# Kernel optimization log

Measured on AMD Instinct MI355X. Metric: run time of the kernel, lower is better.

The kernel has to match this reference:

```python
import jax, jax.numpy as jnp
import numpy as np

N_NODES = 100000
N_EDGES = 1250000
N_PAIRS = 200000
IN_DIM = 128
HID = 64
N_LAYERS = 3


def setup_inputs() -> dict:
    key = jax.random.key(0)
    ks = jax.random.split(key, 16)
    x = jax.random.normal(ks[0], (N_NODES, IN_DIM), dtype=jnp.float32)
    edge_index = jax.random.randint(ks[1], (2, N_EDGES), 0, N_NODES, dtype=jnp.int64)
    pair_index = jax.random.randint(ks[2], (N_PAIRS, 2), 0, N_NODES, dtype=jnp.int64)
    s_in = 1.0 / np.sqrt(IN_DIM)
    s_h = 1.0 / np.sqrt(HID)
    s_2h = 1.0 / np.sqrt(2 * HID)
    enc_W = jax.random.uniform(ks[3], (IN_DIM, HID), jnp.float32, -s_in, s_in)
    enc_b = jax.random.uniform(ks[4], (HID,), jnp.float32, -s_in, s_in)
    # SAGEConv params per layer: lin_l (neighbors, with bias), lin_r (root, no bias)
    Wl = jax.random.uniform(ks[5], (N_LAYERS, HID, HID), jnp.float32, -s_h, s_h)
    bl = jax.random.uniform(ks[6], (N_LAYERS, HID), jnp.float32, -s_h, s_h)
    Wr = jax.random.uniform(ks[7], (N_LAYERS, HID, HID), jnp.float32, -s_h, s_h)
    # predictor MLP: Linear(2h -> h), ReLU, Linear(h -> 1)
    W1 = jax.random.uniform(ks[8], (2 * HID, HID), jnp.float32, -s_2h, s_2h)
    b1 = jax.random.uniform(ks[9], (HID,), jnp.float32, -s_2h, s_2h)
    W2 = jax.random.uniform(ks[10], (HID, 1), jnp.float32, -s_h, s_h)
    b2 = jax.random.uniform(ks[11], (1,), jnp.float32, -s_h, s_h)
    return {"x": x, "edge_index": edge_index, "pair_index": pair_index,
            "enc_W": enc_W, "enc_b": enc_b, "Wl": Wl, "bl": bl, "Wr": Wr,
            "W1": W1, "b1": b1, "W2": W2, "b2": b2}


def reference(x, edge_index, pair_index, enc_W, enc_b, Wl, bl, Wr, W1, b1, W2, b2):
    src, dst = edge_index[0], edge_index[1]
    n = x.shape[0]
    # neighbor counts for mean aggregation (empty neighborhoods -> 0, matching PyG)
    deg = jax.ops.segment_sum(jnp.ones((src.shape[0],), x.dtype), dst, num_segments=n)
    inv_deg = jnp.where(deg > 0, 1.0 / jnp.maximum(deg, 1.0), 0.0)[:, None]  # [N,1]
    # node encoder: Linear + ReLU
    h = jax.nn.relu(x @ enc_W + enc_b)  # [N, HID]
    for i in range(Wl.shape[0]):
        # scatter-mean of source features onto destinations
        agg = jax.ops.segment_sum(h[src], dst, num_segments=n) * inv_deg  # [N, HID]
        h = jax.nn.relu(agg @ Wl[i] + bl[i] + h @ Wr[i])
        # dropout is identity in eval mode
    z = jnp.concatenate([h[pair_index[:, 0]], h[pair_index[:, 1]]], axis=1)  # [P, 2*HID]
    out = (jax.nn.relu(z @ W1 + b1) @ W2 + b2)[:, 0]  # [P]
    return out
```

## Files before the change

kernel.cpp:

```cpp
#include <hip/hip_runtime.h>
#include <hip/hip_fp16.h>
#include <cstdint>
#include <cstddef>

#define N_NODES_C 100000
#define N_EDGES_C 1250000
#define N_PAIRS_C 200000
#define IN_DIM_C 128
#define HID_C 64

#define NB_S 256
#define BSH 9
#define NPB 512
#define NBKT 196
#define SEG_CAP 8192

typedef _Float16 f16x8 __attribute__((ext_vector_type(8)));
typedef float f32x4 __attribute__((ext_vector_type(4)));


#define SCAN_TPB 256
#define SCAN_IPT 4
#define SCAN_ELEMS 1024

__global__ void k_scan_partial(const int* __restrict__ in, int* __restrict__ outp,
                               int* __restrict__ blocksums, int n) {
    __shared__ int sd[SCAN_TPB];
    int tid = threadIdx.x;
    int base = blockIdx.x * SCAN_ELEMS + tid * SCAN_IPT;
    int v[SCAN_IPT]; int s = 0;
    for (int k = 0; k < SCAN_IPT; k++) { int idx = base + k; v[k] = (idx < n) ? in[idx] : 0; s += v[k]; }
    sd[tid] = s;
    __syncthreads();
    for (int off = 1; off < SCAN_TPB; off <<= 1) {
        int t = (tid >= off) ? sd[tid - off] : 0;
        __syncthreads();
        sd[tid] += t;
        __syncthreads();
    }
    int excl = sd[tid] - s;
    for (int k = 0; k < SCAN_IPT; k++) { int idx = base + k; if (idx < n) outp[idx] = excl; excl += v[k]; }
    if (tid == SCAN_TPB - 1) blocksums[blockIdx.x] = sd[tid];
}

__global__ void k_scan_blocks(int* __restrict__ bs, int nb) {
    __shared__ int sd[128];
    int t = threadIdx.x;
    int v = (t < nb) ? bs[t] : 0;
    sd[t] = v;
    __syncthreads();
    for (int off = 1; off < 128; off <<= 1) {
        int u = (t >= off) ? sd[t - off] : 0;
        __syncthreads();
        sd[t] += u;
        __syncthreads();
    }
    if (t < nb) bs[t] = sd[t] - v;
}

__global__ void k_scan_addg(int* __restrict__ arr, const int* __restrict__ bs, int n) {
    int i = blockIdx.x * blockDim.x + threadIdx.x;
    if (i < n) arr[i] += bs[i >> 10];
}


__global__ __launch_bounds__(256) void k_hist(const int* __restrict__ dst,
                                              int* __restrict__ histT, int e) {
    __shared__ int lh[NBKT];
    int tid = threadIdx.x, k = blockIdx.x;
    if (tid < NBKT) lh[tid] = 0;
    __syncthreads();
    int chunk = (e + NB_S - 1) / NB_S;
    int i0 = k * chunk, i1 = min(i0 + chunk, e);
    for (int i = i0 + tid; i < i1; i += 256) atomicAdd(&lh[dst[i] >> BSH], 1);
    __syncthreads();
    if (tid < NBKT) histT[tid * NB_S + k] = lh[tid];
}

__global__ __launch_bounds__(256) void k_scatter(const int* __restrict__ edges,
                                                 const int* __restrict__ offs,
                                                 int2* __restrict__ staging, int e) {
    __shared__ int cur[NBKT];
    int tid = threadIdx.x, k = blockIdx.x;
    if (tid < NBKT) cur[tid] = offs[tid * NB_S + k];
    __syncthreads();
    int chunk = (e + NB_S - 1) / NB_S;
    int i0 = k * chunk, i1 = min(i0 + chunk, e);
    for (int i = i0 + tid; i < i1; i += 256) {
        int s = edges[i];
        int d = edges[e + i];
        int p = atomicAdd(&cur[d >> BSH], 1);
        staging[p] = make_int2(s, d);
    }
}

__global__ __launch_bounds__(256) void k_bucket_fill(const int2* __restrict__ staging,
        const int* __restrict__ offs, int* __restrict__ rowptr,
        float* __restrict__ invd, int* __restrict__ adj, int n, int e) {
    __shared__ int ldeg[NPB];
    __shared__ int lrow[NPB];
    __shared__ int ps[256];
    __shared__ int lseg[SEG_CAP];
    int tid = threadIdx.x, b = blockIdx.x;
    int n0 = b << BSH;
    int nn = min(NPB, n - n0);
    int segBeg = offs[b * NB_S];
    int segEnd = (b == NBKT - 1) ? e : offs[(b + 1) * NB_S];

    ldeg[tid] = 0; ldeg[tid + 256] = 0;
    __syncthreads();
    for (int i = segBeg + tid; i < segEnd; i += 256)
        atomicAdd(&ldeg[staging[i].y - n0], 1);
    __syncthreads();

    int a0 = ldeg[2 * tid], a1 = ldeg[2 * tid + 1];
    int s = a0 + a1;
    ps[tid] = s;
    __syncthreads();
    for (int off = 1; off < 256; off <<= 1) {
        int t = (tid >= off) ? ps[tid - off] : 0;
        __syncthreads();
        ps[tid] += t;
        __syncthreads();
    }
    int excl = ps[tid] - s;
    lrow[2 * tid] = excl;
    lrow[2 * tid + 1] = excl + a0;
    __syncthreads();

    for (int j = tid; j < nn; j += 256) {
        rowptr[n0 + j] = segBeg + lrow[j];
        int d = ldeg[j];
        invd[n0 + j] = (d > 0) ? (1.0f / (float)d) : 0.0f;
    }
    if (b == NBKT - 1 && tid == 0) rowptr[n] = e;
    __syncthreads();

    for (int i = segBeg + tid; i < segEnd; i += 256) {
        int2 ed = staging[i];
        int p = atomicAdd(&lrow[ed.y - n0], 1);
        if (p < SEG_CAP) lseg[p] = ed.x;
        else adj[segBeg + p] = ed.x;
    }
    __syncthreads();

    int m = segEnd - segBeg; if (m > SEG_CAP) m = SEG_CAP;
    for (int p = tid; p < m; p += 256) adj[segBeg + p] = lseg[p];
}


__global__ __launch_bounds__(256) void k_aggregate(const int* __restrict__ rowptr,
        const int* __restrict__ adj, const float* __restrict__ invd,
        const __half* __restrict__ hin16, __half* __restrict__ agg16, int n) {
    int wid = threadIdx.x >> 6, lane = threadIdx.x & 63;
    int node0 = (blockIdx.x * 4 + wid) * 8;
    if (node0 >= n) return;
    const int q = lane >> 3;
    const int c8 = (lane & 7) * 8;
    int node = node0 + q;
    bool valid = node < n;
    int nodec = valid ? node : n - 1;
    int beg = rowptr[nodec], end = rowptr[nodec + 1];
    float a0 = 0.f, a1 = 0.f, a2 = 0.f, a3 = 0.f;
    float a4 = 0.f, a5 = 0.f, a6 = 0.f, a7 = 0.f;
    for (int e = beg; e < end; e += 8) {
        int idx[8];
        #pragma unroll
        for (int j = 0; j < 8; ++j) {
            int ee = e + j;
            idx[j] = adj[ee < end ? ee : end - 1];
        }
        float4 raw[8];
        #pragma unroll
        for (int j = 0; j < 8; ++j)
            raw[j] = *(const float4*)&hin16[(size_t)idx[j] * HID_C + c8];
        #pragma unroll
        for (int j = 0; j < 8; ++j) {
            union { float4 f; __half2 h[4]; } u;
            u.f = raw[j];
            float2 f0 = __half22float2(u.h[0]);
            float2 f1 = __half22float2(u.h[1]);
            float2 f2 = __half22float2(u.h[2]);
            float2 f3 = __half22float2(u.h[3]);
            bool in = (e + j < end);
            a0 += in ? f0.x : 0.f;  a1 += in ? f0.y : 0.f;
            a2 += in ? f1.x : 0.f;  a3 += in ? f1.y : 0.f;
            a4 += in ? f2.x : 0.f;  a5 += in ? f2.y : 0.f;
            a6 += in ? f3.x : 0.f;  a7 += in ? f3.y : 0.f;
        }
    }
    if (valid) {
        float s = invd[node];
        union { float4 f; __half2 h[4]; } o;
        o.h[0] = __floats2half2_rn(a0 * s, a1 * s);
        o.h[1] = __floats2half2_rn(a2 * s, a3 * s);
        o.h[2] = __floats2half2_rn(a4 * s, a5 * s);
        o.h[3] = __floats2half2_rn(a6 * s, a7 * s);
        *(float4*)&agg16[(size_t)node * HID_C + c8] = o.f;
    }
}


__device__ __forceinline__ float4 ld4(const float* p) { return *(const float4*)p; }


template<int SRC>
__global__ __launch_bounds__(256, 2) void k_mm(
    const float* __restrict__ A1f,
    const __half* __restrict__ A1h, const __half* __restrict__ A2h,
    const float* __restrict__ Ws1, const float* __restrict__ Ws2,
    const float* __restrict__ bias,
    __half* __restrict__ out16, int nrows)
{
    __shared__ __half Ah[128 * 128];
    __shared__ __half Bt[64 * 128];
    const int t = threadIdx.x;
    const int g0 = blockIdx.x * 128;

    #pragma unroll
    for (int p = 0; p < 8; ++p) {
        int li = p * 256 + t;
        int r = li >> 4;
        int o = li & 15;
        int g = g0 + r; if (g > nrows - 1) g = nrows - 1;
        f16x8 v;
        if (SRC == 0) {
            const float* src = A1f + (size_t)g * 128 + o * 8;
            float4 f0 = ld4(src), f1 = ld4(src + 4);
            v[0] = (_Float16)f0.x; v[1] = (_Float16)f0.y;
            v[2] = (_Float16)f0.z; v[3] = (_Float16)f0.w;
            v[4] = (_Float16)f1.x; v[5] = (_Float16)f1.y;
            v[6] = (_Float16)f1.z; v[7] = (_Float16)f1.w;
        } else {
            const __half* src = (o < 8) ? (A1h + (size_t)g * 64 + o * 8)
                                        : (A2h + (size_t)g * 64 + (o - 8) * 8);
            v = *(const f16x8*)src;
        }
        *(f16x8*)&Ah[r * 128 + (o ^ (r & 15)) * 8] = v;
    }
    #pragma unroll
    for (int p = 0; p < 32; ++p) {
        int li = p * 256 + t;
        int c = li & 63;
        int k = li >> 6;
        float wv;
        if (SRC == 0) wv = Ws1[k * 64 + c];
        else          wv = (k < 64) ? Ws1[k * 64 + c] : Ws2[(k - 64) * 64 + c];
        Bt[c * 128 + (((k >> 3) ^ (c & 15)) * 8) + (k & 7)] = __float2half(wv);
    }
    __syncthreads();

    const int lane = t & 63;
    const int wid = t >> 6;
    const int R = wid * 32;
    const int lr = lane & 15;
    const int lk = lane >> 4;

    f32x4 acc[2][4];
    #pragma unroll
    for (int fr = 0; fr < 2; ++fr)
        #pragma unroll
        for (int fc = 0; fc < 4; ++fc)
            acc[fr][fc] = (f32x4){0.f, 0.f, 0.f, 0.f};

    #pragma unroll
    for (int ks = 0; ks < 4; ++ks) {
        int o = ks * 4 + lk;
        f16x8 af0, af1;
        {
            int r0 = R + lr;
            int r1 = R + 16 + lr;
            af0 = *(const f16x8*)&Ah[r0 * 128 + (o ^ (r0 & 15)) * 8];
            af1 = *(const f16x8*)&Ah[r1 * 128 + (o ^ (r1 & 15)) * 8];
        }
        #pragma unroll
        for (int fc = 0; fc < 4; ++fc) {
            int c = fc * 16 + lr;
            f16x8 bf = *(const f16x8*)&Bt[c * 128 + (o ^ (c & 15)) * 8];
            acc[0][fc] = __builtin_amdgcn_mfma_f32_16x16x32_f16(af0, bf, acc[0][fc], 0, 0, 0);
            acc[1][fc] = __builtin_amdgcn_mfma_f32_16x16x32_f16(af1, bf, acc[1][fc], 0, 0, 0);
        }
    }

    float bv[4];
    #pragma unroll
    for (int fc = 0; fc < 4; ++fc) bv[fc] = bias[fc * 16 + lr];
    #pragma unroll
    for (int fr = 0; fr < 2; ++fr) {
        #pragma unroll
        for (int j = 0; j < 4; ++j) {
            int gr = g0 + R + fr * 16 + lk * 4 + j;
            if (gr < nrows) {
                #pragma unroll
                for (int fc = 0; fc < 4; ++fc) {
                    int col = fc * 16 + lr;
                    float v = fmaxf(acc[fr][fc][j] + bv[fc], 0.f);
                    out16[(size_t)gr * 64 + col] = __float2half(v);
                }
            }
        }
    }
}


__global__ __launch_bounds__(256, 2) void k_uvm(
    const __half* __restrict__ H16, const float* __restrict__ W1,
    __half* __restrict__ U16, __half* __restrict__ V16, int nrows)
{
    __shared__ __half Ah[128 * 64];
    __shared__ __half Bt[128 * 64];
    const int t = threadIdx.x;
    const int g0 = blockIdx.x * 128;

    #pragma unroll
    for (int p = 0; p < 4; ++p) {
        int li = p * 256 + t;
        int r = li >> 3;
        int o = li & 7;
        int g = g0 + r; if (g > nrows - 1) g = nrows - 1;
        f16x8 v = *(const f16x8*)&H16[(size_t)g * 64 + o * 8];
        *(f16x8*)&Ah[r * 64 + (o ^ (r & 7)) * 8] = v;
    }
    #pragma unroll
    for (int p = 0; p < 32; ++p) {
        int li = p * 256 + t;
        int c = li & 127;
        int k = li >> 7;
        float wv = (c < 64) ? W1[k * 64 + c] : W1[(64 + k) * 64 + (c - 64)];
        Bt[c * 64 + (((k >> 3) ^ (c & 7)) * 8) + (k & 7)] = __float2half(wv);
    }
    __syncthreads();

    const int lane = t & 63;
    const int wid = t >> 6;
    const int R = wid * 32;
    const int lr = lane & 15;
    const int lk = lane >> 4;

    f32x4 acc[2][8];
    #pragma unroll
    for (int fr = 0; fr < 2; ++fr)
        #pragma unroll
        for (int fc = 0; fc < 8; ++fc)
            acc[fr][fc] = (f32x4){0.f, 0.f, 0.f, 0.f};

    #pragma unroll
    for (int ks = 0; ks < 2; ++ks) {
        int o = ks * 4 + lk;
        int r0 = R + lr, r1 = R + 16 + lr;
        f16x8 af0 = *(const f16x8*)&Ah[r0 * 64 + (o ^ (r0 & 7)) * 8];
        f16x8 af1 = *(const f16x8*)&Ah[r1 * 64 + (o ^ (r1 & 7)) * 8];
        #pragma unroll
        for (int fc = 0; fc < 8; ++fc) {
            int c = fc * 16 + lr;
            f16x8 bf = *(const f16x8*)&Bt[c * 64 + (o ^ (c & 7)) * 8];
            acc[0][fc] = __builtin_amdgcn_mfma_f32_16x16x32_f16(af0, bf, acc[0][fc], 0, 0, 0);
            acc[1][fc] = __builtin_amdgcn_mfma_f32_16x16x32_f16(af1, bf, acc[1][fc], 0, 0, 0);
        }
    }

    #pragma unroll
    for (int fr = 0; fr < 2; ++fr) {
        #pragma unroll
        for (int j = 0; j < 4; ++j) {
            int gr = g0 + R + fr * 16 + lk * 4 + j;
            if (gr < nrows) {
                #pragma unroll
                for (int fc = 0; fc < 8; ++fc) {
                    int col = fc * 16 + lr;
                    __half v = __float2half(acc[fr][fc][j]);
                    if (col < 64) U16[(size_t)gr * 64 + col] = v;
                    else          V16[(size_t)gr * 64 + (col - 64)] = v;
                }
            }
        }
    }
}

__global__ __launch_bounds__(256) void k_pred(
    const __half* __restrict__ U16, const __half* __restrict__ V16,
    const int* __restrict__ pidx, const float* __restrict__ b1,
    const float* __restrict__ W2, const float* __restrict__ b2,
    float* __restrict__ outp, int np)
{
    const int t = threadIdx.x;
    const int lg = t & 15;
    const int p = blockIdx.x * 16 + (t >> 4);
    float4 bv = ld4(b1 + lg * 4);
    float4 wv = ld4(W2 + lg * 4);
    if (p >= np) return;
    int2 ab = ((const int2*)pidx)[p];
    float2 ur = *(const float2*)&U16[(size_t)ab.x * 64 + lg * 4];
    float2 vr = *(const float2*)&V16[(size_t)ab.y * 64 + lg * 4];
    union { float f; __half2 h; } u0, u1, v0, v1;
    u0.f = ur.x; u1.f = ur.y; v0.f = vr.x; v1.f = vr.y;
    float2 ua = __half22float2(u0.h), ub = __half22float2(u1.h);
    float2 va = __half22float2(v0.h), vb = __half22float2(v1.h);
    float zx = fmaxf(ua.x + va.x + bv.x, 0.f);
    float zy = fmaxf(ua.y + va.y + bv.y, 0.f);
    float zz = fmaxf(ub.x + vb.x + bv.z, 0.f);
    float zw = fmaxf(ub.y + vb.y + bv.w, 0.f);
    float s = zx * wv.x + zy * wv.y + zz * wv.z + zw * wv.w;
    s += __shfl_down(s, 8, 16);
    s += __shfl_down(s, 4, 16);
    s += __shfl_down(s, 2, 16);
    s += __shfl_down(s, 1, 16);
    if (lg == 0) outp[p] = s + b2[0];
}


extern "C" void kernel_launch(void* const* d_in, const int* in_sizes, int n_in,
                              void* d_out, int out_size, void* d_ws, size_t ws_size,
                              hipStream_t stream) {
    const float* x    = (const float*)d_in[0];
    const int*   edges= (const int*)d_in[1];
    const int*   pair = (const int*)d_in[2];
    const float* encW = (const float*)d_in[3];
    const float* encb = (const float*)d_in[4];
    const float* Wl   = (const float*)d_in[5];
    const float* bl   = (const float*)d_in[6];
    const float* Wr   = (const float*)d_in[7];
    const float* W1   = (const float*)d_in[8];
    const float* b1   = (const float*)d_in[9];
    const float* W2   = (const float*)d_in[10];
    const float* b2   = (const float*)d_in[11];
    float* out = (float*)d_out;

    const int N = N_NODES_C, E = N_EDGES_C, P = N_PAIRS_C;
    const int* dst = edges + E;
    const int M = NBKT * NB_S;

    char* w = (char*)d_ws;
    auto alloc = [&](size_t bytes) { char* p = w; w += (bytes + 255) & ~(size_t)255; return p; };
    int*   rowptr = (int*)alloc((size_t)(N + 1) * 4);
    int*   histT  = (int*)alloc((size_t)M * 4);
    int*   offs   = (int*)alloc((size_t)M * 4);
    int*   bsums  = (int*)alloc(128 * 4);
    float* invd   = (float*)alloc((size_t)N * 4);
    int*   adj    = (int*)alloc((size_t)E * 4);
    int2*  staging= (int2*)alloc((size_t)E * 8);
    __half* h16a  = (__half*)alloc((size_t)N * HID_C * 2);
    __half* h16b  = (__half*)alloc((size_t)N * HID_C * 2);
    __half* agg16 = (__half*)alloc((size_t)N * HID_C * 2);
    __half* U16   = (__half*)alloc((size_t)N * HID_C * 2);
    __half* V16   = (__half*)alloc((size_t)N * HID_C * 2);

    int nscan = (M + SCAN_ELEMS - 1) / SCAN_ELEMS;

    hipLaunchKernelGGL(k_hist, dim3(NB_S), dim3(256), 0, stream, dst, histT, E);
    hipLaunchKernelGGL(k_scan_partial, dim3(nscan), dim3(SCAN_TPB), 0, stream, histT, offs, bsums, M);
    hipLaunchKernelGGL(k_scan_blocks, dim3(1), dim3(128), 0, stream, bsums, nscan);
    hipLaunchKernelGGL(k_scan_addg, dim3((M + 255) / 256), dim3(256), 0, stream, offs, bsums, M);
    hipLaunchKernelGGL(k_scatter, dim3(NB_S), dim3(256), 0, stream, edges, offs, staging, E);
    hipLaunchKernelGGL(k_bucket_fill, dim3(NBKT), dim3(256), 0, stream, staging, offs, rowptr, invd, adj, N, E);

    const int NB128 = (N + 127) / 128;

    k_mm<0><<<dim3(NB128), dim3(256), 0, stream>>>(
        x, nullptr, nullptr, encW, nullptr, encb, h16a, N);

    __half* h16c = h16a; __half* h16n = h16b;
    for (int l = 0; l < 3; l++) {
        hipLaunchKernelGGL(k_aggregate, dim3((N + 31) / 32), dim3(256), 0, stream,
                           rowptr, adj, invd, h16c, agg16, N);
        k_mm<1><<<dim3(NB128), dim3(256), 0, stream>>>(
            nullptr, agg16, h16c, Wl + (size_t)l * 64 * 64, Wr + (size_t)l * 64 * 64,
            bl + (size_t)l * 64, h16n, N);
        __half* t16 = h16c; h16c = h16n; h16n = t16;
    }

    const int NB_UV = (N + 127) / 128;
    hipLaunchKernelGGL(k_uvm, dim3(NB_UV), dim3(256), 0, stream, h16c, W1, U16, V16, N);
    hipLaunchKernelGGL(k_pred, dim3((P + 15) / 16), dim3(256), 0, stream,
                       U16, V16, pair, b1, W2, b2, out, P);
}
```

Baseline: 303.0 us.

## Fuse last SAGE layer with predictor U/V projection and single-block scan

Replaces the three-kernel prefix scan with a single 1024-thread block scan, removing two launches. Fuses the final SAGE layer's matmul (agg·Wl + h·Wr + bias, ReLU) with the W1 split projection into one kernel. The intermediate h stays in shared memory instead of being written to and reread from global. The single-block scan serialises roughly 50K elements on one CU, which may cost more than the launches it removes.

```diff
diff --git a/kernel.cpp b/kernel.cpp
--- a/kernel.cpp
+++ b/kernel.cpp
@@ -19,48 +19,27 @@
 typedef float f32x4 __attribute__((ext_vector_type(4)));
 
 
-#define SCAN_TPB 256
-#define SCAN_IPT 4
-#define SCAN_ELEMS 1024
-
-__global__ void k_scan_partial(const int* __restrict__ in, int* __restrict__ outp,
-                               int* __restrict__ blocksums, int n) {
-    __shared__ int sd[SCAN_TPB];
+__global__ __launch_bounds__(1024) void k_scan_full(const int* __restrict__ in,
+                                                    int* __restrict__ outp, int n) {
+    __shared__ int sd[1024];
     int tid = threadIdx.x;
-    int base = blockIdx.x * SCAN_ELEMS + tid * SCAN_IPT;
-    int v[SCAN_IPT]; int s = 0;
-    for (int k = 0; k < SCAN_IPT; k++) { int idx = base + k; v[k] = (idx < n) ? in[idx] : 0; s += v[k]; }
+    int ipt = (n + 1023) >> 10;
+    int base = tid * ipt;
+    int s = 0;
+    for (int k = 0; k < ipt; ++k) { int idx = base + k; if (idx < n) s += in[idx]; }
     sd[tid] = s;
     __syncthreads();
-    for (int off = 1; off < SCAN_TPB; off <<= 1) {
-        int t = (tid >= off) ? sd[tid - off] : 0;
+    for (int off = 1; off < 1024; off <<= 1) {
+        int tv = (tid >= off) ? sd[tid - off] : 0;
         __syncthreads();
-        sd[tid] += t;
+        sd[tid] += tv;
         __syncthreads();
     }
     int excl = sd[tid] - s;
-    for (int k = 0; k < SCAN_IPT; k++) { int idx = base + k; if (idx < n) outp[idx] = excl; excl += v[k]; }
-    if (tid == SCAN_TPB - 1) blocksums[blockIdx.x] = sd[tid];
-}
-
-__global__ void k_scan_blocks(int* __restrict__ bs, int nb) {
-    __shared__ int sd[128];
-    int t = threadIdx.x;
-    int v = (t < nb) ? bs[t] : 0;
-    sd[t] = v;
-    __syncthreads();
-    for (int off = 1; off < 128; off <<= 1) {
-        int u = (t >= off) ? sd[t - off] : 0;
-        __syncthreads();
-        sd[t] += u;
-        __syncthreads();
-    }
-    if (t < nb) bs[t] = sd[t] - v;
-}
-
-__global__ void k_scan_addg(int* __restrict__ arr, const int* __restrict__ bs, int n) {
-    int i = blockIdx.x * blockDim.x + threadIdx.x;
-    if (i < n) arr[i] += bs[i >> 10];
+    for (int k = 0; k < ipt; ++k) {
+        int idx = base + k;
+        if (idx < n) { int v = in[idx]; outp[idx] = excl; excl += v; }
+    }
 }
 
 
@@ -303,31 +282,35 @@
 }
 
 
-__global__ __launch_bounds__(256, 2) void k_uvm(
-    const __half* __restrict__ H16, const float* __restrict__ W1,
+__global__ __launch_bounds__(256, 2) void k_mm_uv(
+    const __half* __restrict__ A1h, const __half* __restrict__ A2h,
+    const float* __restrict__ Ws1, const float* __restrict__ Ws2,
+    const float* __restrict__ bias, const float* __restrict__ W1p,
     __half* __restrict__ U16, __half* __restrict__ V16, int nrows)
 {
-    __shared__ __half Ah[128 * 64];
-    __shared__ __half Bt[128 * 64];
+    __shared__ __half Ah[128 * 128];
+    __shared__ __half Bt[64 * 128];
     const int t = threadIdx.x;
     const int g0 = blockIdx.x * 128;
 
     #pragma unroll
-    for (int p = 0; p < 4; ++p) {
+    for (int p = 0; p < 8; ++p) {
         int li = p * 256 + t;
-        int r = li >> 3;
-        int o = li & 7;
+        int r = li >> 4;
+        int o = li & 15;
         int g = g0 + r; if (g > nrows - 1) g = nrows - 1;
-        f16x8 v = *(const f16x8*)&H16[(size_t)g * 64 + o * 8];
-        *(f16x8*)&Ah[r * 64 + (o ^ (r & 7)) * 8] = v;
+        const __half* src = (o < 8) ? (A1h + (size_t)g * 64 + o * 8)
+                                    : (A2h + (size_t)g * 64 + (o - 8) * 8);
+        f16x8 v = *(const f16x8*)src;
+        *(f16x8*)&Ah[r * 128 + (o ^ (r & 15)) * 8] = v;
     }
     #pragma unroll
     for (int p = 0; p < 32; ++p) {
         int li = p * 256 + t;
-        int c = li & 127;
-        int k = li >> 7;
-        float wv = (c < 64) ? W1[k * 64 + c] : W1[(64 + k) * 64 + (c - 64)];
-        Bt[c * 64 + (((k >> 3) ^ (c & 7)) * 8) + (k & 7)] = __float2half(wv);
+        int c = li & 63;
+        int k = li >> 6;
+        float wv = (k < 64) ? Ws1[k * 64 + c] : Ws2[(k - 64) * 64 + c];
+        Bt[c * 128 + (((k >> 3) ^ (c & 15)) * 8) + (k & 7)] = __float2half(wv);
     }
     __syncthreads();
 
@@ -337,12 +320,64 @@
     const int lr = lane & 15;
     const int lk = lane >> 4;
 
-    f32x4 acc[2][8];
+    f32x4 acc[2][4];
     #pragma unroll
     for (int fr = 0; fr < 2; ++fr)
         #pragma unroll
+        for (int fc = 0; fc < 4; ++fc)
+            acc[fr][fc] = (f32x4){0.f, 0.f, 0.f, 0.f};
+
+    #pragma unroll
+    for (int ks = 0; ks < 4; ++ks) {
+        int o = ks * 4 + lk;
+        int r0 = R + lr, r1 = R + 16 + lr;
+        f16x8 af0 = *(const f16x8*)&Ah[r0 * 128 + (o ^ (r0 & 15)) * 8];
+        f16x8 af1 = *(const f16x8*)&Ah[r1 * 128 + (o ^ (r1 & 15)) * 8];
+        #pragma unroll
+        for (int fc = 0; fc < 4; ++fc) {
+            int c = fc * 16 + lr;
+            f16x8 bf = *(const f16x8*)&Bt[c * 128 + (o ^ (c & 15)) * 8];
+            acc[0][fc] = __builtin_amdgcn_mfma_f32_16x16x32_f16(af0, bf, acc[0][fc], 0, 0, 0);
+            acc[1][fc] = __builtin_amdgcn_mfma_f32_16x16x32_f16(af1, bf, acc[1][fc], 0, 0, 0);
+        }
+    }
+
+    float bv[4];
+    #pragma unroll
+    for (int fc = 0; fc < 4; ++fc) bv[fc] = bias[fc * 16 + lr];
+
+    __syncthreads();
+
+    #pragma unroll
+    for (int fr = 0; fr < 2; ++fr) {
+        #pragma unroll
+        for (int j = 0; j < 4; ++j) {
+            int lrow = R + fr * 16 + lk * 4 + j;
+            #pragma unroll
+            for (int fc = 0; fc < 4; ++fc) {
+                int col = fc * 16 + lr;
+                float v = fmaxf(acc[fr][fc][j] + bv[fc], 0.f);
+                int o = col >> 3;
+                Ah[lrow * 64 + ((o ^ (lrow & 7)) * 8) + (col & 7)] = __float2half(v);
+            }
+        }
+    }
+    #pragma unroll
+    for (int p = 0; p < 32; ++p) {
+        int li = p * 256 + t;
+        int c = li & 127;
+        int k = li >> 7;
+        float wv = (c < 64) ? W1p[k * 64 + c] : W1p[(64 + k) * 64 + (c - 64)];
+        Bt[c * 64 + (((k >> 3) ^ (c & 7)) * 8) + (k & 7)] = __float2half(wv);
+    }
+    __syncthreads();
+
+    f32x4 acc2[2][8];
+    #pragma unroll
+    for (int fr = 0; fr < 2; ++fr)
+        #pragma unroll
         for (int fc = 0; fc < 8; ++fc)
-            acc[fr][fc] = (f32x4){0.f, 0.f, 0.f, 0.f};
+            acc2[fr][fc] = (f32x4){0.f, 0.f, 0.f, 0.f};
 
     #pragma unroll
     for (int ks = 0; ks < 2; ++ks) {
@@ -354,8 +389,8 @@
         for (int fc = 0; fc < 8; ++fc) {
             int c = fc * 16 + lr;
             f16x8 bf = *(const f16x8*)&Bt[c * 64 + (o ^ (c & 7)) * 8];
-            acc[0][fc] = __builtin_amdgcn_mfma_f32_16x16x32_f16(af0, bf, acc[0][fc], 0, 0, 0);
-            acc[1][fc] = __builtin_amdgcn_mfma_f32_16x16x32_f16(af1, bf, acc[1][fc], 0, 0, 0);
+            acc2[0][fc] = __builtin_amdgcn_mfma_f32_16x16x32_f16(af0, bf, acc2[0][fc], 0, 0, 0);
+            acc2[1][fc] = __builtin_amdgcn_mfma_f32_16x16x32_f16(af1, bf, acc2[1][fc], 0, 0, 0);
         }
     }
 
@@ -368,7 +403,7 @@
                 #pragma unroll
                 for (int fc = 0; fc < 8; ++fc) {
                     int col = fc * 16 + lr;
-                    __half v = __float2half(acc[fr][fc][j]);
+                    __half v = __float2half(acc2[fr][fc][j]);
                     if (col < 64) U16[(size_t)gr * 64 + col] = v;
                     else          V16[(size_t)gr * 64 + (col - 64)] = v;
                 }
@@ -435,7 +470,6 @@
     int*   rowptr = (int*)alloc((size_t)(N + 1) * 4);
     int*   histT  = (int*)alloc((size_t)M * 4);
     int*   offs   = (int*)alloc((size_t)M * 4);
-    int*   bsums  = (int*)alloc(128 * 4);
     float* invd   = (float*)alloc((size_t)N * 4);
     int*   adj    = (int*)alloc((size_t)E * 4);
     int2*  staging= (int2*)alloc((size_t)E * 8);
@@ -445,12 +479,8 @@
     __half* U16   = (__half*)alloc((size_t)N * HID_C * 2);
     __half* V16   = (__half*)alloc((size_t)N * HID_C * 2);
 
-    int nscan = (M + SCAN_ELEMS - 1) / SCAN_ELEMS;
-
     hipLaunchKernelGGL(k_hist, dim3(NB_S), dim3(256), 0, stream, dst, histT, E);
-    hipLaunchKernelGGL(k_scan_partial, dim3(nscan), dim3(SCAN_TPB), 0, stream, histT, offs, bsums, M);
-    hipLaunchKernelGGL(k_scan_blocks, dim3(1), dim3(128), 0, stream, bsums, nscan);
-    hipLaunchKernelGGL(k_scan_addg, dim3((M + 255) / 256), dim3(256), 0, stream, offs, bsums, M);
+    hipLaunchKernelGGL(k_scan_full, dim3(1), dim3(1024), 0, stream, histT, offs, M);
     hipLaunchKernelGGL(k_scatter, dim3(NB_S), dim3(256), 0, stream, edges, offs, staging, E);
     hipLaunchKernelGGL(k_bucket_fill, dim3(NBKT), dim3(256), 0, stream, staging, offs, rowptr, invd, adj, N, E);
 
@@ -460,7 +490,7 @@
         x, nullptr, nullptr, encW, nullptr, encb, h16a, N);
 
     __half* h16c = h16a; __half* h16n = h16b;
-    for (int l = 0; l < 3; l++) {
+    for (int l = 0; l < 2; l++) {
         hipLaunchKernelGGL(k_aggregate, dim3((N + 31) / 32), dim3(256), 0, stream,
                            rowptr, adj, invd, h16c, agg16, N);
         k_mm<1><<<dim3(NB128), dim3(256), 0, stream>>>(
@@ -469,8 +499,12 @@
         __half* t16 = h16c; h16c = h16n; h16n = t16;
     }
 
-    const int NB_UV = (N + 127) / 128;
-    hipLaunchKernelGGL(k_uvm, dim3(NB_UV), dim3(256), 0, stream, h16c, W1, U16, V16, N);
+    hipLaunchKernelGGL(k_aggregate, dim3((N + 31) / 32), dim3(256), 0, stream,
+                       rowptr, adj, invd, h16c, agg16, N);
+    hipLaunchKernelGGL(k_mm_uv, dim3(NB128), dim3(256), 0, stream,
+                       agg16, h16c, Wl + (size_t)2 * 64 * 64, Wr + (size_t)2 * 64 * 64,
+                       bl + (size_t)2 * 64, W1, U16, V16, N);
+
     hipLaunchKernelGGL(k_pred, dim3((P + 15) / 16), dim3(256), 0, stream,
                        U16, V16, pair, b1, W2, b2, out, P);
 }
```

Measured after the change: 384.4 us. +26.9%, slower.
